# Optimization experiments

Hardware: AMD Instinct MI355X
Metric: run time of the kernel (lower is better)

Reference implementation:

```python
import jax, jax.numpy as jnp
import numpy as np

INPUT_SIZE = 12288  # C*H*W = 3*64*64
HIDDEN = 1024
OUT_SHAPE = (3, 64, 64)
T_STEPS = 256


def setup_inputs() -> dict:
    key = jax.random.key(0)
    ks = jax.random.split(key, 7)
    s = 0.02
    frames = jax.random.normal(ks[0], (T_STEPS, *OUT_SHAPE), dtype=jnp.float32)
    W_ih = jax.random.normal(ks[1], (4 * HIDDEN, INPUT_SIZE), dtype=jnp.float32) * s
    W_hh = jax.random.normal(ks[2], (4 * HIDDEN, HIDDEN), dtype=jnp.float32) * s
    b_ih = jax.random.normal(ks[3], (4 * HIDDEN,), dtype=jnp.float32) * s
    b_hh = jax.random.normal(ks[4], (4 * HIDDEN,), dtype=jnp.float32) * s
    fc_w = jax.random.normal(ks[5], (INPUT_SIZE, HIDDEN), dtype=jnp.float32) * s
    fc_b = jax.random.normal(ks[6], (INPUT_SIZE,), dtype=jnp.float32) * s
    return {"frames": frames, "W_ih": W_ih, "W_hh": W_hh, "b_ih": b_ih,
            "b_hh": b_hh, "fc_w": fc_w, "fc_b": fc_b, "T": T_STEPS}


def _lstm_scan(x_flat, W_ih, W_hh, b_ih, b_hh):
    # Precompute input projections for all timesteps in one GEMM: (T, 4H)
    x_proj = x_flat @ W_ih.T + b_ih + b_hh
    H = W_hh.shape[1]

    def step(carry, xp):
        h, c = carry  # (H,), (H,)
        gates = xp + h @ W_hh.T  # (4H,)
        i = jax.nn.sigmoid(gates[0 * H:1 * H])
        f = jax.nn.sigmoid(gates[1 * H:2 * H])
        g = jnp.tanh(gates[2 * H:3 * H])
        o = jax.nn.sigmoid(gates[3 * H:4 * H])
        c_new = f * c + i * g
        h_new = o * jnp.tanh(c_new)
        return (h_new, c_new), None

    init = (jnp.zeros((H,), x_flat.dtype), jnp.zeros((H,), x_flat.dtype))
    (h_T, _), _ = jax.lax.scan(step, init, x_proj)
    return h_T


def reference(frames, W_ih, W_hh, b_ih, b_hh, fc_w, fc_b, T):
    Tn, C, Hh, Ww = frames.shape
    x_flat = frames.reshape(Tn, -1)  # (T, C*H*W)
    h_T = _lstm_scan(x_flat, W_ih, W_hh, b_ih, b_hh)  # (HIDDEN,)
    context = h_T @ fc_w.T + fc_b  # (C*H*W,)
    return context.reshape(1, C, Hh, Ww)
```

## Files before the change

kernel.cpp:

```cpp
#include <hip/hip_runtime.h>
#include <math.h>

#define K_IN 12288
#define HID  1024
#define G4   4096
#define TS   256

typedef unsigned long long u64;
typedef unsigned int u32;

#define GBM 128
#define GBN 128
#define GBK 16
#define LDG 132

#define MAC44(ACC, A, B)                                                     \
  ACC[0][0] += A.x * B.x; ACC[0][1] += A.x * B.y;                            \
  ACC[0][2] += A.x * B.z; ACC[0][3] += A.x * B.w;                            \
  ACC[1][0] += A.y * B.x; ACC[1][1] += A.y * B.y;                            \
  ACC[1][2] += A.y * B.z; ACC[1][3] += A.y * B.w;                            \
  ACC[2][0] += A.z * B.x; ACC[2][1] += A.z * B.y;                            \
  ACC[2][2] += A.z * B.z; ACC[2][3] += A.z * B.w;                            \
  ACC[3][0] += A.w * B.x; ACC[3][1] += A.w * B.y;                            \
  ACC[3][2] += A.w * B.z; ACC[3][3] += A.w * B.w;

__global__ __launch_bounds__(256, 2) void xproj_gemm(
    const float* __restrict__ X,
    const float* __restrict__ W,
    float* __restrict__ xpart,
    int kspan)
{
  __shared__ float As[GBK][LDG];
  __shared__ float Bs[GBK][LDG];
  const int tid = threadIdx.x;
  const int t0 = blockIdx.x * GBN;
  const int j0 = blockIdx.y * GBM;
  const int ks = blockIdx.z;
  const int kbeg = ks * kspan;
  const int kend = kbeg + kspan;

  const int tx = tid & 15;
  const int ty = tid >> 4;
  const int ca0 = tx * 4, ca1 = 64 + tx * 4;
  const int cb0 = ty * 4, cb1 = 64 + ty * 4;

  const int r0 = tid >> 2;
  const int kq = tid & 3;

  float acc[2][2][4][4];
#pragma unroll
  for (int ia = 0; ia < 2; ++ia)
#pragma unroll
    for (int ib = 0; ib < 2; ++ib)
#pragma unroll
      for (int a = 0; a < 4; ++a)
#pragma unroll
        for (int b = 0; b < 4; ++b) acc[ia][ib][a][b] = 0.f;

  float4 a0v = *(const float4*)(W + (size_t)(j0 + r0) * K_IN + kbeg + kq * 4);
  float4 a1v = *(const float4*)(W + (size_t)(j0 + 64 + r0) * K_IN + kbeg + kq * 4);
  float4 b0v = *(const float4*)(X + (size_t)(t0 + r0) * K_IN + kbeg + kq * 4);
  float4 b1v = *(const float4*)(X + (size_t)(t0 + 64 + r0) * K_IN + kbeg + kq * 4);

  for (int k0 = kbeg; k0 < kend; k0 += GBK) {
    __syncthreads();
    As[kq * 4 + 0][r0] = a0v.x; As[kq * 4 + 1][r0] = a0v.y;
    As[kq * 4 + 2][r0] = a0v.z; As[kq * 4 + 3][r0] = a0v.w;
    As[kq * 4 + 0][64 + r0] = a1v.x; As[kq * 4 + 1][64 + r0] = a1v.y;
    As[kq * 4 + 2][64 + r0] = a1v.z; As[kq * 4 + 3][64 + r0] = a1v.w;
    Bs[kq * 4 + 0][r0] = b0v.x; Bs[kq * 4 + 1][r0] = b0v.y;
    Bs[kq * 4 + 2][r0] = b0v.z; Bs[kq * 4 + 3][r0] = b0v.w;
    Bs[kq * 4 + 0][64 + r0] = b1v.x; Bs[kq * 4 + 1][64 + r0] = b1v.y;
    Bs[kq * 4 + 2][64 + r0] = b1v.z; Bs[kq * 4 + 3][64 + r0] = b1v.w;
    __syncthreads();

    const int kn = k0 + GBK;
    if (kn < kend) {
      a0v = *(const float4*)(W + (size_t)(j0 + r0) * K_IN + kn + kq * 4);
      a1v = *(const float4*)(W + (size_t)(j0 + 64 + r0) * K_IN + kn + kq * 4);
      b0v = *(const float4*)(X + (size_t)(t0 + r0) * K_IN + kn + kq * 4);
      b1v = *(const float4*)(X + (size_t)(t0 + 64 + r0) * K_IN + kn + kq * 4);
    }

#pragma unroll
    for (int kk = 0; kk < GBK; ++kk) {
      float4 a0 = *(const float4*)&As[kk][ca0];
      float4 a1 = *(const float4*)&As[kk][ca1];
      float4 b0 = *(const float4*)&Bs[kk][cb0];
      float4 b1 = *(const float4*)&Bs[kk][cb1];
      MAC44(acc[0][0], a0, b0);
      MAC44(acc[0][1], a0, b1);
      MAC44(acc[1][0], a1, b0);
      MAC44(acc[1][1], a1, b1);
    }
  }

  float* outp = xpart + (size_t)ks * TS * G4;
#pragma unroll
  for (int ib = 0; ib < 2; ++ib) {
    const int tb = t0 + (ib ? cb1 : cb0);
#pragma unroll
    for (int y = 0; y < 4; ++y) {
#pragma unroll
      for (int ia = 0; ia < 2; ++ia) {
        float4 o;
        o.x = acc[ia][ib][0][y]; o.y = acc[ia][ib][1][y];
        o.z = acc[ia][ib][2][y]; o.w = acc[ia][ib][3][y];
        *(float4*)(outp + (size_t)(tb + y) * G4 + j0 + (ia ? ca1 : ca0)) = o;
      }
    }
  }
}

__global__ __launch_bounds__(256) void xproj_reduce(
    const float* __restrict__ xpart, int nks,
    const float* __restrict__ b_ih, const float* __restrict__ b_hh,
    float* __restrict__ xproj)
{
  const int idx = (blockIdx.x * 256 + threadIdx.x) * 4;
  float4 s = *(const float4*)(xpart + idx);
  for (int ks = 1; ks < nks; ++ks) {
    float4 p = *(const float4*)(xpart + (size_t)ks * TS * G4 + idx);
    s.x += p.x; s.y += p.y; s.z += p.z; s.w += p.w;
  }
  const int j = idx & (G4 - 1);
  float4 bi = *(const float4*)(b_ih + j);
  float4 bh = *(const float4*)(b_hh + j);
  s.x += bi.x + bh.x; s.y += bi.y + bh.y; s.z += bi.z + bh.z; s.w += bi.w + bh.w;
  *(float4*)(xproj + idx) = s;
}

#define NWG 128
#define UPW 8

__global__ __launch_bounds__(256, 1) void lstm_scan(
    const float* __restrict__ W_hh,
    const float* __restrict__ xproj,
    u64* __restrict__ hmsg)
{
  const int tid = threadIdx.x;
  const int w = blockIdx.x;
  const int u0 = w * UPW;
  const int r = tid >> 3;
  const int sub = tid & 7;
  const int gate = r >> 3;
  const int uu = r & 7;
  const int hrow = gate * HID + u0 + uu;

  __shared__ __align__(16) float h_lds[8 * 132];
  __shared__ float gates_lds[32];
  __shared__ float c_lds[UPW];

  float4 Wreg[32];
  const float4* wp = (const float4*)(W_hh + (size_t)hrow * HID + sub * 128);
#pragma unroll
  for (int i = 0; i < 32; ++i) Wreg[i] = wp[i];

  if (tid < UPW) c_lds[tid] = 0.f;
  __syncthreads();

  for (int t = 0; t < TS; ++t) {
    float xp = 0.f;
    if (sub == 0) xp = xproj[(size_t)t * G4 + hrow];

    float partial = 0.f;
    if (t > 0) {
      const u64* slot = hmsg + (t & 1) * HID;
      const u32 tt = (u32)t;
      u64 m0, m1, m2, m3;
      do {
        m0 = __hip_atomic_load(&slot[tid * 4 + 0], __ATOMIC_RELAXED,
                               __HIP_MEMORY_SCOPE_AGENT);
      } while ((u32)(m0 >> 32) != tt);
      m1 = __hip_atomic_load(&slot[tid * 4 + 1], __ATOMIC_RELAXED,
                             __HIP_MEMORY_SCOPE_AGENT);
      m2 = __hip_atomic_load(&slot[tid * 4 + 2], __ATOMIC_RELAXED,
                             __HIP_MEMORY_SCOPE_AGENT);
      m3 = __hip_atomic_load(&slot[tid * 4 + 3], __ATOMIC_RELAXED,
                             __HIP_MEMORY_SCOPE_AGENT);
      while ((u32)(m1 >> 32) != tt)
        m1 = __hip_atomic_load(&slot[tid * 4 + 1], __ATOMIC_RELAXED,
                               __HIP_MEMORY_SCOPE_AGENT);
      while ((u32)(m2 >> 32) != tt)
        m2 = __hip_atomic_load(&slot[tid * 4 + 2], __ATOMIC_RELAXED,
                               __HIP_MEMORY_SCOPE_AGENT);
      while ((u32)(m3 >> 32) != tt)
        m3 = __hip_atomic_load(&slot[tid * 4 + 3], __ATOMIC_RELAXED,
                               __HIP_MEMORY_SCOPE_AGENT);
      __syncthreads();
      const int st = tid >> 5;
      const int off = (tid & 31) * 4;
      h_lds[st * 132 + off + 0] = __uint_as_float((u32)m0);
      h_lds[st * 132 + off + 1] = __uint_as_float((u32)m1);
      h_lds[st * 132 + off + 2] = __uint_as_float((u32)m2);
      h_lds[st * 132 + off + 3] = __uint_as_float((u32)m3);
      __syncthreads();
      const float4* hl = (const float4*)(h_lds + sub * 132);
#pragma unroll
      for (int i = 0; i < 32; ++i) {
        float4 h4 = hl[i];
        partial += Wreg[i].x * h4.x + Wreg[i].y * h4.y +
                   Wreg[i].z * h4.z + Wreg[i].w * h4.w;
      }
    }
    partial += __shfl_xor(partial, 1, 64);
    partial += __shfl_xor(partial, 2, 64);
    partial += __shfl_xor(partial, 4, 64);
    if (sub == 0) {
      float gsum = partial + xp;
      float act = (gate == 2) ? tanhf(gsum) : 1.f / (1.f + expf(-gsum));
      gates_lds[gate * 8 + uu] = act;
    }
    __syncthreads();
    if (tid < UPW) {
      float iv = gates_lds[0 * 8 + tid];
      float fv = gates_lds[1 * 8 + tid];
      float gv = gates_lds[2 * 8 + tid];
      float ov = gates_lds[3 * 8 + tid];
      float c = fv * c_lds[tid] + iv * gv;
      c_lds[tid] = c;
      float hnew = ov * tanhf(c);
      u64 msg = ((u64)(u32)(t + 1) << 32) | (u64)__float_as_uint(hnew);
      __hip_atomic_store(&hmsg[((t + 1) & 1) * HID + u0 + tid], msg,
                         __ATOMIC_RELAXED, __HIP_MEMORY_SCOPE_AGENT);
    }
  }
}

__global__ __launch_bounds__(256) void fc_kernel(
    const float* __restrict__ fc_w,
    const float* __restrict__ fc_b,
    const u64* __restrict__ hmsg,
    float* __restrict__ out)
{
  __shared__ float h_s[HID];
  const int tid = threadIdx.x;
  for (int k = tid; k < HID; k += 256)
    h_s[k] = __uint_as_float((u32)hmsg[k]);
  __syncthreads();
  const int r = tid >> 2;
  const int sub = tid & 3;
  const int j = blockIdx.x * 64 + r;
  const float4* wrow = (const float4*)(fc_w + (size_t)j * HID + sub * 256);
  const float4* hp = (const float4*)(h_s + sub * 256);
  float s = 0.f;
#pragma unroll
  for (int i = 0; i < 64; ++i) {
    float4 wv = wrow[i];
    float4 hv = hp[i];
    s += wv.x * hv.x + wv.y * hv.y + wv.z * hv.z + wv.w * hv.w;
  }
  s += __shfl_xor(s, 1, 64);
  s += __shfl_xor(s, 2, 64);
  if (sub == 0) out[j] = s + fc_b[j];
}

extern "C" void kernel_launch(void* const* d_in, const int* in_sizes, int n_in,
                              void* d_out, int out_size, void* d_ws, size_t ws_size,
                              hipStream_t stream) {
  const float* frames = (const float*)d_in[0];
  const float* W_ih   = (const float*)d_in[1];
  const float* W_hh   = (const float*)d_in[2];
  const float* b_ih   = (const float*)d_in[3];
  const float* b_hh   = (const float*)d_in[4];
  const float* fc_w   = (const float*)d_in[5];
  const float* fc_b   = (const float*)d_in[6];
  float* out = (float*)d_out;

  const size_t XPROJ_BYTES = (size_t)TS * G4 * 4;
  int nks = 1;
  if (ws_size >= XPROJ_BYTES * 9 + (1 << 20)) nks = 8;
  else if (ws_size >= XPROJ_BYTES * 5 + (1 << 20)) nks = 4;
  else if (ws_size >= XPROJ_BYTES * 3 + (1 << 20)) nks = 2;

  char* ws = (char*)d_ws;
  float* xproj = (float*)ws;
  float* xpart = (float*)(ws + XPROJ_BYTES);
  u64*   hmsg  = (u64*)(ws + XPROJ_BYTES * (1 + nks));

  const int kspan = K_IN / nks;
  xproj_gemm<<<dim3(TS / GBN, G4 / GBM, nks), 256, 0, stream>>>(frames, W_ih, xpart, kspan);
  xproj_reduce<<<dim3(TS * G4 / 4 / 256), 256, 0, stream>>>(xpart, nks, b_ih, b_hh, xproj);
  lstm_scan<<<dim3(NWG), 256, 0, stream>>>(W_hh, xproj, hmsg);
  fc_kernel<<<dim3(12288 / 64), 256, 0, stream>>>(fc_w, fc_b, hmsg, out);
}
```

Measured before the change: 1.209 ms.

## Use split-fp16 MFMA for input projection GEMM with transposed output layout

The FP32 SIMT tiled GEMM computing the input projections is replaced with MFMA 32x32x16 fp16 instructions. Each operand is split into high and low fp16 parts and three products are accumulated to approximate fp32 accuracy. The output is written transposed (gate-major, time-minor), so the scan kernel reads each gate row contiguously over time. This targets the compute-bound GEMM at the cost of 3x MFMA work, fp16 range/precision risk, and strided scalar output stores.

Result: faster. 1.023 ms (-15.4%).

```diff
diff --git a/kernel.cpp b/kernel.cpp
--- a/kernel.cpp
+++ b/kernel.cpp
@@ -8,126 +8,145 @@
 
 typedef unsigned long long u64;
 typedef unsigned int u32;
-
-#define GBM 128
-#define GBN 128
-#define GBK 16
-#define LDG 132
-
-#define MAC44(ACC, A, B)                                                     \
-  ACC[0][0] += A.x * B.x; ACC[0][1] += A.x * B.y;                            \
-  ACC[0][2] += A.x * B.z; ACC[0][3] += A.x * B.w;                            \
-  ACC[1][0] += A.y * B.x; ACC[1][1] += A.y * B.y;                            \
-  ACC[1][2] += A.y * B.z; ACC[1][3] += A.y * B.w;                            \
-  ACC[2][0] += A.z * B.x; ACC[2][1] += A.z * B.y;                            \
-  ACC[2][2] += A.z * B.z; ACC[2][3] += A.z * B.w;                            \
-  ACC[3][0] += A.w * B.x; ACC[3][1] += A.w * B.y;                            \
-  ACC[3][2] += A.w * B.z; ACC[3][3] += A.w * B.w;
-
-__global__ __launch_bounds__(256, 2) void xproj_gemm(
+typedef __attribute__((ext_vector_type(4))) float f32x4;
+typedef __attribute__((ext_vector_type(16))) float f32x16;
+typedef __attribute__((ext_vector_type(8))) _Float16 half8;
+typedef __attribute__((ext_vector_type(4))) _Float16 half4;
+
+__global__ __launch_bounds__(512, 2) void xproj_gemm(
     const float* __restrict__ X,
     const float* __restrict__ W,
-    float* __restrict__ xpart,
+    float* __restrict__ xpartT,
     int kspan)
 {
-  __shared__ float As[GBK][LDG];
-  __shared__ float Bs[GBK][LDG];
+  __shared__ __align__(16) _Float16 Ahi[2][128][8];
+  __shared__ __align__(16) _Float16 Alo[2][128][8];
+  __shared__ __align__(16) _Float16 Bhi[2][256][8];
+  __shared__ __align__(16) _Float16 Blo[2][256][8];
+
   const int tid = threadIdx.x;
-  const int t0 = blockIdx.x * GBN;
-  const int j0 = blockIdx.y * GBM;
-  const int ks = blockIdx.z;
+  const int wave = tid >> 6;
+  const int lane = tid & 63;
+  const int l31 = lane & 31;
+  const int kh = lane >> 5;
+
+  const int j0 = blockIdx.x * 128;
+  const int ks = blockIdx.y;
   const int kbeg = ks * kspan;
-  const int kend = kbeg + kspan;
-
-  const int tx = tid & 15;
-  const int ty = tid >> 4;
-  const int ca0 = tx * 4, ca1 = 64 + tx * 4;
-  const int cb0 = ty * 4, cb1 = 64 + ty * 4;
-
-  const int r0 = tid >> 2;
-  const int kq = tid & 3;
-
-  float acc[2][2][4][4];
-#pragma unroll
-  for (int ia = 0; ia < 2; ++ia)
-#pragma unroll
-    for (int ib = 0; ib < 2; ++ib)
-#pragma unroll
-      for (int a = 0; a < 4; ++a)
-#pragma unroll
-        for (int b = 0; b < 4; ++b) acc[ia][ib][a][b] = 0.f;
-
-  float4 a0v = *(const float4*)(W + (size_t)(j0 + r0) * K_IN + kbeg + kq * 4);
-  float4 a1v = *(const float4*)(W + (size_t)(j0 + 64 + r0) * K_IN + kbeg + kq * 4);
-  float4 b0v = *(const float4*)(X + (size_t)(t0 + r0) * K_IN + kbeg + kq * 4);
-  float4 b1v = *(const float4*)(X + (size_t)(t0 + 64 + r0) * K_IN + kbeg + kq * 4);
-
-  for (int k0 = kbeg; k0 < kend; k0 += GBK) {
+
+  const int jw = (wave & 1) * 64;
+  const int tw = (wave >> 1) * 64;
+
+  const int wrow = tid >> 2;
+  const int wkq  = tid & 3;
+  const int xrow = tid >> 1;
+  const int xkq  = tid & 1;
+
+  const float* wsrc = W + (size_t)(j0 + wrow) * K_IN + kbeg + wkq * 4;
+  const float* xsrc = X + (size_t)xrow * K_IN + kbeg + xkq * 8;
+
+  f32x16 acc[2][2];
+#pragma unroll
+  for (int mi = 0; mi < 2; ++mi)
+#pragma unroll
+    for (int ni = 0; ni < 2; ++ni)
+#pragma unroll
+      for (int e = 0; e < 16; ++e) acc[mi][ni][e] = 0.f;
+
+  f32x4 wv  = *(const f32x4*)wsrc;
+  f32x4 xv0 = *(const f32x4*)xsrc;
+  f32x4 xv1 = *(const f32x4*)(xsrc + 4);
+
+  const int nsteps = kspan >> 4;
+  for (int s = 0; s < nsteps; ++s) {
+    {
+      half4 hw, lw;
+#pragma unroll
+      for (int e = 0; e < 4; ++e) {
+        _Float16 h = (_Float16)wv[e];
+        hw[e] = h;
+        lw[e] = (_Float16)(wv[e] - (float)h);
+      }
+      *(half4*)&Ahi[wkq >> 1][wrow][(wkq & 1) * 4] = hw;
+      *(half4*)&Alo[wkq >> 1][wrow][(wkq & 1) * 4] = lw;
+      half8 hx, lx;
+#pragma unroll
+      for (int e = 0; e < 4; ++e) {
+        _Float16 h0 = (_Float16)xv0[e];
+        hx[e] = h0;
+        lx[e] = (_Float16)(xv0[e] - (float)h0);
+        _Float16 h1 = (_Float16)xv1[e];
+        hx[e + 4] = h1;
+        lx[e + 4] = (_Float16)(xv1[e] - (float)h1);
+      }
+      *(half8*)&Bhi[xkq][xrow][0] = hx;
+      *(half8*)&Blo[xkq][xrow][0] = lx;
+    }
     __syncthreads();
-    As[kq * 4 + 0][r0] = a0v.x; As[kq * 4 + 1][r0] = a0v.y;
-    As[kq * 4 + 2][r0] = a0v.z; As[kq * 4 + 3][r0] = a0v.w;
-    As[kq * 4 + 0][64 + r0] = a1v.x; As[kq * 4 + 1][64 + r0] = a1v.y;
-    As[kq * 4 + 2][64 + r0] = a1v.z; As[kq * 4 + 3][64 + r0] = a1v.w;
-    Bs[kq * 4 + 0][r0] = b0v.x; Bs[kq * 4 + 1][r0] = b0v.y;
-    Bs[kq * 4 + 2][r0] = b0v.z; Bs[kq * 4 + 3][r0] = b0v.w;
-    Bs[kq * 4 + 0][64 + r0] = b1v.x; Bs[kq * 4 + 1][64 + r0] = b1v.y;
-    Bs[kq * 4 + 2][64 + r0] = b1v.z; Bs[kq * 4 + 3][64 + r0] = b1v.w;
+
+    if (s + 1 < nsteps) {
+      const int ko = (s + 1) * 16;
+      wv  = *(const f32x4*)(wsrc + ko);
+      xv0 = *(const f32x4*)(xsrc + ko);
+      xv1 = *(const f32x4*)(xsrc + ko + 4);
+    }
+
+    half8 aH[2], aL[2], bH[2], bL[2];
+#pragma unroll
+    for (int mi = 0; mi < 2; ++mi) {
+      aH[mi] = *(const half8*)&Ahi[kh][jw + mi * 32 + l31][0];
+      aL[mi] = *(const half8*)&Alo[kh][jw + mi * 32 + l31][0];
+    }
+#pragma unroll
+    for (int ni = 0; ni < 2; ++ni) {
+      bH[ni] = *(const half8*)&Bhi[kh][tw + ni * 32 + l31][0];
+      bL[ni] = *(const half8*)&Blo[kh][tw + ni * 32 + l31][0];
+    }
+
+    acc[0][0] = __builtin_amdgcn_mfma_f32_32x32x16_f16(aH[0], bH[0], acc[0][0], 0, 0, 0);
+    acc[0][1] = __builtin_amdgcn_mfma_f32_32x32x16_f16(aH[0], bH[1], acc[0][1], 0, 0, 0);
+    acc[1][0] = __builtin_amdgcn_mfma_f32_32x32x16_f16(aH[1], bH[0], acc[1][0], 0, 0, 0);
+    acc[1][1] = __builtin_amdgcn_mfma_f32_32x32x16_f16(aH[1], bH[1], acc[1][1], 0, 0, 0);
+    acc[0][0] = __builtin_amdgcn_mfma_f32_32x32x16_f16(aH[0], bL[0], acc[0][0], 0, 0, 0);
+    acc[0][1] = __builtin_amdgcn_mfma_f32_32x32x16_f16(aH[0], bL[1], acc[0][1], 0, 0, 0);
+    acc[1][0] = __builtin_amdgcn_mfma_f32_32x32x16_f16(aH[1], bL[0], acc[1][0], 0, 0, 0);
+    acc[1][1] = __builtin_amdgcn_mfma_f32_32x32x16_f16(aH[1], bL[1], acc[1][1], 0, 0, 0);
+    acc[0][0] = __builtin_amdgcn_mfma_f32_32x32x16_f16(aL[0], bH[0], acc[0][0], 0, 0, 0);
+    acc[0][1] = __builtin_amdgcn_mfma_f32_32x32x16_f16(aL[0], bH[1], acc[0][1], 0, 0, 0);
+    acc[1][0] = __builtin_amdgcn_mfma_f32_32x32x16_f16(aL[1], bH[0], acc[1][0], 0, 0, 0);
+    acc[1][1] = __builtin_amdgcn_mfma_f32_32x32x16_f16(aL[1], bH[1], acc[1][1], 0, 0, 0);
+
     __syncthreads();
-
-    const int kn = k0 + GBK;
-    if (kn < kend) {
-      a0v = *(const float4*)(W + (size_t)(j0 + r0) * K_IN + kn + kq * 4);
-      a1v = *(const float4*)(W + (size_t)(j0 + 64 + r0) * K_IN + kn + kq * 4);
-      b0v = *(const float4*)(X + (size_t)(t0 + r0) * K_IN + kn + kq * 4);
-      b1v = *(const float4*)(X + (size_t)(t0 + 64 + r0) * K_IN + kn + kq * 4);
-    }
-
-#pragma unroll
-    for (int kk = 0; kk < GBK; ++kk) {
-      float4 a0 = *(const float4*)&As[kk][ca0];
-      float4 a1 = *(const float4*)&As[kk][ca1];
-      float4 b0 = *(const float4*)&Bs[kk][cb0];
-      float4 b1 = *(const float4*)&Bs[kk][cb1];
-      MAC44(acc[0][0], a0, b0);
-      MAC44(acc[0][1], a0, b1);
-      MAC44(acc[1][0], a1, b0);
-      MAC44(acc[1][1], a1, b1);
-    }
   }
 
-  float* outp = xpart + (size_t)ks * TS * G4;
-#pragma unroll
-  for (int ib = 0; ib < 2; ++ib) {
-    const int tb = t0 + (ib ? cb1 : cb0);
-#pragma unroll
-    for (int y = 0; y < 4; ++y) {
-#pragma unroll
-      for (int ia = 0; ia < 2; ++ia) {
-        float4 o;
-        o.x = acc[ia][ib][0][y]; o.y = acc[ia][ib][1][y];
-        o.z = acc[ia][ib][2][y]; o.w = acc[ia][ib][3][y];
-        *(float4*)(outp + (size_t)(tb + y) * G4 + j0 + (ia ? ca1 : ca0)) = o;
+  float* outp = xpartT + (size_t)ks * G4 * TS;
+#pragma unroll
+  for (int mi = 0; mi < 2; ++mi)
+#pragma unroll
+    for (int ni = 0; ni < 2; ++ni)
+#pragma unroll
+      for (int rg = 0; rg < 16; ++rg) {
+        const int j = j0 + jw + mi * 32 + (rg & 3) + 8 * (rg >> 2) + 4 * kh;
+        const int t = tw + ni * 32 + l31;
+        outp[(size_t)j * TS + t] = acc[mi][ni][rg];
       }
-    }
-  }
 }
 
 __global__ __launch_bounds__(256) void xproj_reduce(
-    const float* __restrict__ xpart, int nks,
+    const float* __restrict__ xpartT, int nks,
     const float* __restrict__ b_ih, const float* __restrict__ b_hh,
-    float* __restrict__ xproj)
+    float* __restrict__ xprojT)
 {
   const int idx = (blockIdx.x * 256 + threadIdx.x) * 4;
-  float4 s = *(const float4*)(xpart + idx);
+  float4 s = *(const float4*)(xpartT + idx);
   for (int ks = 1; ks < nks; ++ks) {
-    float4 p = *(const float4*)(xpart + (size_t)ks * TS * G4 + idx);
+    float4 p = *(const float4*)(xpartT + (size_t)ks * G4 * TS + idx);
     s.x += p.x; s.y += p.y; s.z += p.z; s.w += p.w;
   }
-  const int j = idx & (G4 - 1);
-  float4 bi = *(const float4*)(b_ih + j);
-  float4 bh = *(const float4*)(b_hh + j);
-  s.x += bi.x + bh.x; s.y += bi.y + bh.y; s.z += bi.z + bh.z; s.w += bi.w + bh.w;
-  *(float4*)(xproj + idx) = s;
+  const int j = idx >> 8;
+  const float bias = b_ih[j] + b_hh[j];
+  s.x += bias; s.y += bias; s.z += bias; s.w += bias;
+  *(float4*)(xprojT + idx) = s;
 }
 
 #define NWG 128
@@ -135,7 +154,7 @@
 
 __global__ __launch_bounds__(256, 1) void lstm_scan(
     const float* __restrict__ W_hh,
-    const float* __restrict__ xproj,
+    const float* __restrict__ xprojT,
     u64* __restrict__ hmsg)
 {
   const int tid = threadIdx.x;
@@ -156,12 +175,14 @@
 #pragma unroll
   for (int i = 0; i < 32; ++i) Wreg[i] = wp[i];
 
+  const float* xrow = xprojT + (size_t)hrow * TS;
+
   if (tid < UPW) c_lds[tid] = 0.f;
   __syncthreads();
 
   for (int t = 0; t < TS; ++t) {
     float xp = 0.f;
-    if (sub == 0) xp = xproj[(size_t)t * G4 + hrow];
+    if (sub == 0) xp = xrow[t];
 
     float partial = 0.f;
     if (t > 0) {
@@ -274,13 +295,13 @@
   else if (ws_size >= XPROJ_BYTES * 3 + (1 << 20)) nks = 2;
 
   char* ws = (char*)d_ws;
-  float* xproj = (float*)ws;
-  float* xpart = (float*)(ws + XPROJ_BYTES);
-  u64*   hmsg  = (u64*)(ws + XPROJ_BYTES * (1 + nks));
+  float* xprojT = (float*)ws;
+  float* xpartT = (float*)(ws + XPROJ_BYTES);
+  u64*   hmsg   = (u64*)(ws + XPROJ_BYTES * (1 + nks));
 
   const int kspan = K_IN / nks;
-  xproj_gemm<<<dim3(TS / GBN, G4 / GBM, nks), 256, 0, stream>>>(frames, W_ih, xpart, kspan);
-  xproj_reduce<<<dim3(TS * G4 / 4 / 256), 256, 0, stream>>>(xpart, nks, b_ih, b_hh, xproj);
-  lstm_scan<<<dim3(NWG), 256, 0, stream>>>(W_hh, xproj, hmsg);
+  xproj_gemm<<<dim3(G4 / 128, nks), 512, 0, stream>>>(frames, W_ih, xpartT, kspan);
+  xproj_reduce<<<dim3(G4 * TS / 4 / 256), 256, 0, stream>>>(xpartT, nks, b_ih, b_hh, xprojT);
+  lstm_scan<<<dim3(NWG), 256, 0, stream>>>(W_hh, xprojT, hmsg);
   fc_kernel<<<dim3(12288 / 64), 256, 0, stream>>>(fc_w, fc_b, hmsg, out);
 }
```
